# Kernel tuning notes

Measured on AMD Instinct MI355X. Metric: run time of the kernel, lower is better.

Reference implementation:

```python
import jax, jax.numpy as jnp
import numpy as np

B, T0, J = 32, 2048, 128
C, T_L = 512, 16


def setup_inputs() -> dict:
    key = jax.random.key(0)
    k1, k2, k3, k4, k5 = jax.random.split(key, 5)
    x = jax.random.normal(k1, (B, T0, J), dtype=jnp.float32)
    lens = jax.random.randint(k2, (B,), 0, T0 - T_L)  # ensure idx stays in-range
    sos = jax.random.normal(k3, (J,), dtype=jnp.float32)
    label_seqs = jax.random.uniform(k4, (C, T_L, J), dtype=jnp.float32)
    W = jax.random.normal(k5, (J, J), dtype=jnp.float32) / np.sqrt(J)
    return {"x": x, "lens": lens, "sos": sos, "label_seqs": label_seqs, "W": W}


def _similarity(pred_seq, labels):
    # per-neuron squared-error similarity, averaged over J: [B,Tl,J],[C,Tl,J] -> [B,C,Tl]
    p2 = jnp.sum(pred_seq * pred_seq, axis=-1)          # [B,Tl]
    l2 = jnp.sum(labels * labels, axis=-1)              # [C,Tl]
    cross = jnp.einsum('btj,ctj->bct', pred_seq, labels)
    return (p2[:, None, :] + l2[None, :, :] - 2.0 * cross) / pred_seq.shape[-1]


def reference(x, lens, sos, label_seqs, W):
    b_ar = jnp.arange(B)
    sos_b = jnp.broadcast_to(sos, (B, J))
    # place sos at position lens[b], then prepend sos (vectorized scatter)
    x = x.at[b_ar, lens].set(sos_b)
    x = jnp.concatenate([sos_b[:, None, :], x], axis=1)  # [B, T0+1, J]
    idx2d = jnp.arange(T_L)[None, :] + lens[:, None] + 1  # [B, T_l]

    def gather_pred(xc):
        pred = jnp.einsum('btj,jk->btk', xc, W)          # stub search_forward
        return pred[b_ar[:, None], idx2d]                # [B, T_l, J]

    pls = gather_pred(x)
    sim0 = _similarity(pls[:, :1, :], label_seqs[:, :1, :])  # [B,C,1]
    sofar = jnp.argmin(sim0[:, :, 0], axis=-1)               # [B]

    def body(t, carry):
        xc, sofar, _ = carry
        lab = label_seqs[sofar]                              # [B, T_l, J]
        xc = xc.at[b_ar[:, None], idx2d].set(lab)            # fused scatter update
        pls = gather_pred(xc)
        sim = _similarity(pls, label_seqs)                   # [B, C, T_l]
        mask = (jnp.arange(T_L) < t).astype(sim.dtype)
        sim_mean = jnp.sum(sim * mask, axis=-1) / t
        sofar = jnp.argmin(sim_mean, axis=-1)
        return (xc, sofar, pls)

    _, sofar, pls = jax.lax.fori_loop(1, T_L + 1, body, (x, sofar, pls))
    return sofar, pls
```

## Files before the change

kernel.cpp:

```cpp
#include <hip/hip_runtime.h>

#define Jd   128
#define Cn   512
#define TLn  16
#define Bn   32


__device__ __forceinline__ unsigned int f2ord(float f) {
    unsigned int u = __float_as_uint(f);
    return (u & 0x80000000u) ? ~u : (u | 0x80000000u);
}
__device__ __forceinline__ unsigned long long packkey(float v, int c) {
    return ((unsigned long long)f2ord(v) << 32) | (unsigned int)c;
}

__global__ void k_prep2(const float* __restrict__ L, const float* __restrict__ W,
                        float* __restrict__ LT, float* __restrict__ l2T,
                        float* __restrict__ PLT) {
    __shared__ float Ls[32][132];
    __shared__ float Ws[32][128];
    int tid = threadIdx.x, bid = blockIdx.x;
    int tau = bid & 15, c0 = (bid >> 4) * 32;

    int r = tid >> 3, o = tid & 7;
    const float4* src = (const float4*)(L + ((size_t)(c0 + r) * TLn + tau) * Jd);
    float l2p = 0.f;
    #pragma unroll
    for (int i = 0; i < 4; ++i) {
        float4 v = src[o * 4 + i];
        *(float4*)&Ls[r][(o * 4 + i) * 4] = v;
        l2p += v.x * v.x + v.y * v.y + v.z * v.z + v.w * v.w;
    }
    l2p += __shfl_xor(l2p, 1, 64);
    l2p += __shfl_xor(l2p, 2, 64);
    l2p += __shfl_xor(l2p, 4, 64);
    if (o == 0) l2T[tau * Cn + c0 + r] = l2p;
    __syncthreads();
    int cc = tid & 31, jg = tid >> 5;
    #pragma unroll
    for (int j = jg; j < Jd; j += 8)
        LT[((size_t)tau * Jd + j) * Cn + c0 + cc] = Ls[cc][j];

    int ch = tid & 31, jh = tid >> 5;
    float acc[4][4] = {};
    for (int kb = 0; kb < 4; ++kb) {
        __syncthreads();
        int kk = tid >> 3, oo = tid & 7;
        const float4* wsrc = (const float4*)(W + (size_t)(kb * 32 + kk) * Jd);
        #pragma unroll
        for (int i = 0; i < 4; ++i)
            *(float4*)&Ws[kk][(oo * 4 + i) * 4] = wsrc[oo * 4 + i];
        __syncthreads();
        #pragma unroll 8
        for (int k = 0; k < 32; ++k) {
            float lv = Ls[ch][kb * 32 + k];
            #pragma unroll
            for (int it = 0; it < 4; ++it) {
                float4 wv = *(const float4*)&Ws[k][it * 32 + jh * 4];
                acc[it][0] = fmaf(lv, wv.x, acc[it][0]);
                acc[it][1] = fmaf(lv, wv.y, acc[it][1]);
                acc[it][2] = fmaf(lv, wv.z, acc[it][2]);
                acc[it][3] = fmaf(lv, wv.w, acc[it][3]);
            }
        }
    }
    #pragma unroll
    for (int it = 0; it < 4; ++it)
        #pragma unroll
        for (int u = 0; u < 4; ++u) {
            int j = it * 32 + jh * 4 + u;
            PLT[((size_t)tau * Jd + j) * Cn + c0 + ch] = acc[it][u];
        }
}

__global__ void __launch_bounds__(256, 2)
k_dot(const float* __restrict__ LT, const float* __restrict__ PLT,
      const float* __restrict__ l2T,
      const float* __restrict__ sos, const float* __restrict__ W,
      float* __restrict__ DOT, float* __restrict__ S0) {
    __shared__ float As[64][64];
    __shared__ float Bs[64][128];
    int tid = threadIdx.x, bid = blockIdx.x;

    if (bid == 512) {
        float* pred0 = &As[0][0];
        if (tid < Jd) {
            float a = 0.f;
            for (int k = 0; k < Jd; ++k) a = fmaf(sos[k], W[k * Jd + tid], a);
            pred0[tid] = a;
        }
        __syncthreads();
        float a0 = 0.f, a1 = 0.f;
        for (int jj = 0; jj < Jd; ++jj) {
            float p = pred0[jj];
            float d0 = p - LT[(size_t)jj * Cn + tid];
            float d1 = p - LT[(size_t)jj * Cn + tid + 256];
            a0 = fmaf(d0, d0, a0);
            a1 = fmaf(d1, d1, a1);
        }
        S0[tid] = a0;  S0[tid + 256] = a1;
        return;
    }

    int tau = bid & 15, st = (bid >> 4) & 7, cq = bid >> 7;
    int s0 = st * 64, c0 = cq * 128;
    int sg = tid >> 4, cg = tid & 15;

    float acc[4][8] = {};
    for (int h = 0; h < 2; ++h) {
        __syncthreads();
        const float4* Asrc = (const float4*)(PLT + ((size_t)tau * Jd + h * 64) * Cn + s0);
        #pragma unroll
        for (int i = 0; i < 4; ++i) {
            int flat = i * 256 + tid;
            int row = flat >> 4, col = flat & 15;
            *(float4*)&As[row][col * 4] = Asrc[(size_t)row * (Cn / 4) + col];
        }
        const float4* Bsrc = (const float4*)(LT + ((size_t)tau * Jd + h * 64) * Cn + c0);
        #pragma unroll
        for (int i = 0; i < 8; ++i) {
            int flat = i * 256 + tid;
            int row = flat >> 5, col = flat & 31;
            *(float4*)&Bs[row][col * 4] = Bsrc[(size_t)row * (Cn / 4) + col];
        }
        __syncthreads();
        #pragma unroll 4
        for (int j = 0; j < 64; ++j) {
            float4 a  = *(const float4*)&As[j][sg * 4];
            float4 b0 = *(const float4*)&Bs[j][cg * 4];
            float4 b1 = *(const float4*)&Bs[j][64 + cg * 4];
            float av[4] = {a.x, a.y, a.z, a.w};
            float bv[8] = {b0.x, b0.y, b0.z, b0.w, b1.x, b1.y, b1.z, b1.w};
            #pragma unroll
            for (int i = 0; i < 4; ++i)
                #pragma unroll
                for (int q = 0; q < 8; ++q)
                    acc[i][q] = fmaf(av[i], bv[q], acc[i][q]);
        }
    }

    float4 l2a = *(const float4*)(l2T + tau * Cn + c0 + cg * 4);
    float4 l2b = *(const float4*)(l2T + tau * Cn + c0 + 64 + cg * 4);
    #pragma unroll
    for (int i = 0; i < 4; ++i) {
        int s = s0 + sg * 4 + i;
        float* dst = DOT + ((size_t)s * TLn + tau) * Cn + c0;
        float4 v0 = {l2a.x - 2.f * acc[i][0], l2a.y - 2.f * acc[i][1],
                     l2a.z - 2.f * acc[i][2], l2a.w - 2.f * acc[i][3]};
        float4 v1 = {l2b.x - 2.f * acc[i][4], l2b.y - 2.f * acc[i][5],
                     l2b.z - 2.f * acc[i][6], l2b.w - 2.f * acc[i][7]};
        *(float4*)(dst + cg * 4) = v0;
        *(float4*)(dst + 64 + cg * 4) = v1;
    }
}

__global__ void k_fin(const float* __restrict__ S0, const float* __restrict__ DOT,
                      const float* __restrict__ PLT, float* __restrict__ out) {
    __shared__ unsigned long long red[4];
    __shared__ int sCur;
    __shared__ int keys[TLn + 1];
    int tid = threadIdx.x, w = tid >> 6, lane = tid & 63;

    for (int t = 0; t <= TLn; ++t) {
        float sum0, sum1;
        if (t == 0) {
            sum0 = S0[tid];  sum1 = S0[tid + 256];
        } else {
            const float* base = DOT + (size_t)sCur * TLn * Cn;
            float v0[TLn], v1[TLn];
            #pragma unroll
            for (int tau = 0; tau < TLn; ++tau) {
                v0[tau] = base[(size_t)tau * Cn + tid];
                v1[tau] = base[(size_t)tau * Cn + tid + 256];
            }
            sum0 = sum1 = 0.f;
            #pragma unroll
            for (int tau = 0; tau < TLn; ++tau) {
                float m = (tau < t) ? 1.f : 0.f;
                sum0 = fmaf(v0[tau], m, sum0);
                sum1 = fmaf(v1[tau], m, sum1);
            }
        }
        unsigned long long m0 = packkey(sum0, tid);
        unsigned long long m1 = packkey(sum1, tid + 256);
        unsigned long long m = (m1 < m0) ? m1 : m0;
        for (int o = 32; o; o >>= 1) {
            unsigned long long o2 = __shfl_down(m, o, 64);
            if (o2 < m) m = o2;
        }
        if (lane == 0) red[w] = m;
        __syncthreads();
        if (tid == 0) {
            unsigned long long b = red[0];
            #pragma unroll
            for (int i = 1; i < 4; ++i) if (red[i] < b) b = red[i];
            int sv = (int)(b & 0xFFFFFFFFull);
            sCur = sv;  keys[t] = sv;
        }
        __syncthreads();
    }

    int s16 = keys[TLn], s15 = keys[TLn - 1];
    float v[8];
    #pragma unroll
    for (int q = 0; q < 8; ++q)
        v[q] = PLT[(size_t)(q * 256 + tid) * Cn + s15];
    if (tid < Bn) out[tid] = (float)s16;
    #pragma unroll
    for (int q = 0; q < 8; ++q)
        for (int b = 0; b < Bn; ++b)
            out[Bn + (size_t)b * (TLn * Jd) + q * 256 + tid] = v[q];
}

extern "C" void kernel_launch(void* const* d_in, const int* in_sizes, int n_in,
                              void* d_out, int out_size, void* d_ws, size_t ws_size,
                              hipStream_t stream) {
    const float* sos = (const float*)d_in[2];
    const float* L   = (const float*)d_in[3];
    const float* W   = (const float*)d_in[4];
    float* out = (float*)d_out;

    const size_t l2Off  = 4096;
    const size_t pltOff = 65536;
    const size_t ltOff  = pltOff + (size_t)TLn * Jd * Cn * sizeof(float);
    const size_t dotOff = ltOff  + (size_t)TLn * Jd * Cn * sizeof(float);
    const size_t need   = dotOff + (size_t)Cn * TLn * Cn * sizeof(float);
    char* base = (ws_size >= need) ? (char*)d_ws : (char*)d_in[0];
    float* S0   = (float*)base;
    float* l2T  = (float*)(base + l2Off);
    float* PLT  = (float*)(base + pltOff);
    float* LT   = (float*)(base + ltOff);
    float* DOT  = (float*)(base + dotOff);

    hipLaunchKernelGGL(k_prep2, dim3(256), dim3(256), 0, stream, L, W, LT, l2T, PLT);
    hipLaunchKernelGGL(k_dot,   dim3(513), dim3(256), 0, stream,
                       LT, PLT, l2T, sos, W, DOT, S0);
    hipLaunchKernelGGL(k_fin,   dim3(1),   dim3(256), 0, stream, S0, DOT, PLT, out);
}
```

Measured before the change: 129.0 us.

## Split label-projection prep kernel across output halves for more blocks

The prep kernel that transposes label sequences and projects them through W is restructured. Each block now handles half of the output columns, which doubles the grid to 512 blocks. The block stores labels transposed in shared memory and loads its whole W half at once, so the k-block loop and its repeated barriers are gone. Each thread now holds 8 accumulators instead of 16. The aim is more parallelism and occupancy in a small kernel, at the cost of loading the label tile twice and adding bank-conflict-prone transposed shared stores.

```diff
diff --git a/kernel.cpp b/kernel.cpp
--- a/kernel.cpp
+++ b/kernel.cpp
@@ -14,63 +14,66 @@
     return ((unsigned long long)f2ord(v) << 32) | (unsigned int)c;
 }
 
-__global__ void k_prep2(const float* __restrict__ L, const float* __restrict__ W,
-                        float* __restrict__ LT, float* __restrict__ l2T,
-                        float* __restrict__ PLT) {
-    __shared__ float Ls[32][132];
-    __shared__ float Ws[32][128];
+__global__ void __launch_bounds__(256, 4)
+k_prep3(const float* __restrict__ L, const float* __restrict__ W,
+        float* __restrict__ LT, float* __restrict__ l2T,
+        float* __restrict__ PLT) {
+    __shared__ float Lst[128][36];
+    __shared__ float Ws[128][68];
     int tid = threadIdx.x, bid = blockIdx.x;
-    int tau = bid & 15, c0 = (bid >> 4) * 32;
-
-    int r = tid >> 3, o = tid & 7;
-    const float4* src = (const float4*)(L + ((size_t)(c0 + r) * TLn + tau) * Jd);
+    int tau = bid & 15, jh = (bid >> 4) & 1, c0 = (bid >> 5) * 32;
+    int j0 = jh * 64;
+
+    int cr = tid >> 3, oc = tid & 7;
+    const float4* src = (const float4*)(L + ((size_t)(c0 + cr) * TLn + tau) * Jd);
     float l2p = 0.f;
     #pragma unroll
     for (int i = 0; i < 4; ++i) {
-        float4 v = src[o * 4 + i];
-        *(float4*)&Ls[r][(o * 4 + i) * 4] = v;
+        float4 v = src[oc * 4 + i];
+        int kb = (oc * 4 + i) * 4;
+        Lst[kb + 0][cr] = v.x;  Lst[kb + 1][cr] = v.y;
+        Lst[kb + 2][cr] = v.z;  Lst[kb + 3][cr] = v.w;
         l2p += v.x * v.x + v.y * v.y + v.z * v.z + v.w * v.w;
     }
-    l2p += __shfl_xor(l2p, 1, 64);
-    l2p += __shfl_xor(l2p, 2, 64);
-    l2p += __shfl_xor(l2p, 4, 64);
-    if (o == 0) l2T[tau * Cn + c0 + r] = l2p;
+    l2p += __shfl_down(l2p, 4, 8);
+    l2p += __shfl_down(l2p, 2, 8);
+    l2p += __shfl_down(l2p, 1, 8);
+    if (oc == 0 && jh == 0) l2T[tau * Cn + c0 + cr] = l2p;
+
+    #pragma unroll
+    for (int r = 0; r < 8; ++r) {
+        int idx = r * 256 + tid;
+        int k = idx >> 4, f = idx & 15;
+        *(float4*)&Ws[k][f * 4] = *(const float4*)(W + (size_t)k * Jd + j0 + f * 4);
+    }
     __syncthreads();
-    int cc = tid & 31, jg = tid >> 5;
-    #pragma unroll
-    for (int j = jg; j < Jd; j += 8)
-        LT[((size_t)tau * Jd + j) * Cn + c0 + cc] = Ls[cc][j];
-
-    int ch = tid & 31, jh = tid >> 5;
-    float acc[4][4] = {};
-    for (int kb = 0; kb < 4; ++kb) {
-        __syncthreads();
-        int kk = tid >> 3, oo = tid & 7;
-        const float4* wsrc = (const float4*)(W + (size_t)(kb * 32 + kk) * Jd);
+
+    int c = tid & 31, jq = tid >> 5;
+
+    if (jh == 0) {
         #pragma unroll
-        for (int i = 0; i < 4; ++i)
-            *(float4*)&Ws[kk][(oo * 4 + i) * 4] = wsrc[oo * 4 + i];
-        __syncthreads();
-        #pragma unroll 8
-        for (int k = 0; k < 32; ++k) {
-            float lv = Ls[ch][kb * 32 + k];
-            #pragma unroll
-            for (int it = 0; it < 4; ++it) {
-                float4 wv = *(const float4*)&Ws[k][it * 32 + jh * 4];
-                acc[it][0] = fmaf(lv, wv.x, acc[it][0]);
-                acc[it][1] = fmaf(lv, wv.y, acc[it][1]);
-                acc[it][2] = fmaf(lv, wv.z, acc[it][2]);
-                acc[it][3] = fmaf(lv, wv.w, acc[it][3]);
-            }
-        }
-    }
-    #pragma unroll
-    for (int it = 0; it < 4; ++it)
-        #pragma unroll
-        for (int u = 0; u < 4; ++u) {
-            int j = it * 32 + jh * 4 + u;
-            PLT[((size_t)tau * Jd + j) * Cn + c0 + ch] = acc[it][u];
-        }
+        for (int k = jq; k < Jd; k += 8)
+            LT[((size_t)tau * Jd + k) * Cn + c0 + c] = Lst[k][c];
+    }
+
+    float acc[8] = {};
+    #pragma unroll 4
+    for (int k = 0; k < Jd; ++k) {
+        float a = Lst[k][c];
+        float4 w0 = *(const float4*)&Ws[k][jq * 8];
+        float4 w1 = *(const float4*)&Ws[k][jq * 8 + 4];
+        acc[0] = fmaf(a, w0.x, acc[0]);
+        acc[1] = fmaf(a, w0.y, acc[1]);
+        acc[2] = fmaf(a, w0.z, acc[2]);
+        acc[3] = fmaf(a, w0.w, acc[3]);
+        acc[4] = fmaf(a, w1.x, acc[4]);
+        acc[5] = fmaf(a, w1.y, acc[5]);
+        acc[6] = fmaf(a, w1.z, acc[6]);
+        acc[7] = fmaf(a, w1.w, acc[7]);
+    }
+    #pragma unroll
+    for (int i = 0; i < 8; ++i)
+        PLT[((size_t)tau * Jd + j0 + jq * 8 + i) * Cn + c0 + c] = acc[i];
 }
 
 __global__ void __launch_bounds__(256, 2)
@@ -232,7 +235,7 @@
     float* LT   = (float*)(base + ltOff);
     float* DOT  = (float*)(base + dotOff);
 
-    hipLaunchKernelGGL(k_prep2, dim3(256), dim3(256), 0, stream, L, W, LT, l2T, PLT);
+    hipLaunchKernelGGL(k_prep3, dim3(512), dim3(256), 0, stream, L, W, LT, l2T, PLT);
     hipLaunchKernelGGL(k_dot,   dim3(513), dim3(256), 0, stream,
                        LT, PLT, l2T, sos, W, DOT, S0);
     hipLaunchKernelGGL(k_fin,   dim3(1),   dim3(256), 0, stream, S0, DOT, PLT, out);
```

Result: faster. 125.1 us (-3.0%).
